# Kernel optimization log

Measured on AMD Instinct MI355X. Metric: run time of the kernel, lower is better.

The kernel has to match this reference:

```python
import jax, jax.numpy as jnp
import numpy as np

N, M, D = 500000, 128, 16

def setup_inputs() -> dict:
    key = jax.random.key(0)
    k1, k2, k3 = jax.random.split(key, 3)
    points = jax.random.uniform(k1, (N, D), dtype=jnp.float32)
    centers = jax.random.uniform(k2, (M, D), dtype=jnp.float32)
    # module initializes covs_inv_sqrt = 15*I per center; add small noise so it's non-trivial
    covs_inv_sqrt = 15.0 * jnp.eye(D, dtype=jnp.float32)[None, :, :] \
        + 0.1 * jax.random.normal(k3, (M, D, D), dtype=jnp.float32)
    weights = jnp.ones((M,), dtype=jnp.float32)
    threshold = jnp.zeros((1,), dtype=jnp.float32)
    return {"points": points, "centers": centers, "covs_inv_sqrt": covs_inv_sqrt,
            "weights": weights, "threshold": threshold}

def reference(points, centers, covs_inv_sqrt, weights, threshold):
    # refresh(): covs_inv = L @ L^T per center
    covs_inv = jnp.einsum('jde,jfe->jdf', covs_inv_sqrt, covs_inv_sqrt)  # [M,D,D]
    # equal_clusters=True branch
    w = jnp.abs(weights)
    center_prs = w / (w.sum() + 1e-30)
    coefs = center_prs * jnp.sqrt(jnp.linalg.det(covs_inv))  # [M]
    # Mahalanobis quadratic form (x-c)^T S (x-c) expanded as xSx - 2 xSc + cSc
    S_flat = covs_inv.reshape(M, D * D)                          # [M,D^2]
    xx = (points[:, :, None] * points[:, None, :]).reshape(-1, D * D)  # [N,D^2]
    Sc = jnp.einsum('jde,je->jd', covs_inv, centers)             # [M,D]
    cSc = jnp.einsum('jd,jd->j', centers, Sc)                    # [M]
    q = xx @ S_flat.T - 2.0 * (points @ Sc.T) + cSc[None, :]     # [N,M]
    d_ij = -0.5 * q
    # weighted online logsumexp over centers (KeOps logsumexp with weight Vj(coefs))
    log_lik = jax.nn.logsumexp(d_ij, axis=1, b=coefs[None, :], keepdims=True)  # [N,1]
    return log_lik - threshold
```

## Files before the change

### kernel.cpp

```cpp
#include <hip/hip_runtime.h>
#include <math.h>

#define M_CTR 128
#define D_DIM 16
#define KSTEPS 10
#define NSLOT 80
#define GRID_MAIN 2048
#define LOG2E 1.4426950408889634f
#define LN2   0.6931471805599453f

typedef _Float16 half8  __attribute__((ext_vector_type(8)));
typedef __fp16   fp16x2 __attribute__((ext_vector_type(2)));
typedef float   f32x16  __attribute__((ext_vector_type(16)));

struct SlotTab { unsigned char a[NSLOT]; unsigned char b[NSLOT]; unsigned char m[NSLOT]; };
constexpr SlotTab make_tab() {
    SlotTab T{};
    int s = 0;
    for (int d = 0; d < 8; ++d) { T.a[s] = (unsigned char)d; T.b[s] = (unsigned char)d; T.m[s] = 0; ++s; }
    for (int d = 0; d < 8; ++d)
        for (int f = d + 1; f < 8; ++f) { T.a[s] = (unsigned char)d; T.b[s] = (unsigned char)f; T.m[s] = 0; ++s; }
    for (int d = 0; d < 8; ++d)
        for (int f2 = d + 1; f2 < 8; ++f2) { T.a[s] = (unsigned char)d; T.b[s] = (unsigned char)(f2 + 8); T.m[s] = 0; ++s; }
    for (int d = 0; d < 4; ++d) { T.a[s] = (unsigned char)d; T.b[s] = (unsigned char)(d + 8); T.m[s] = 1; ++s; }
    for (int d = 0; d < 8; ++d) { T.a[s] = (unsigned char)d; T.b[s] = 0; T.m[s] = 2; ++s; }
    for (; s < NSLOT; ++s) { T.a[s] = 0; T.b[s] = 0; T.m[s] = 3; }
    return T;
}
constexpr SlotTab TAB = make_tab();

__global__ __launch_bounds__(64) void gmm_prep_kernel(
    const float* __restrict__ centers,
    const float* __restrict__ Lmat,
    const float* __restrict__ weights,
    float* __restrict__ ws)
{
    const int j    = blockIdx.x;
    const int lane = threadIdx.x;
    const int r    = lane & 15;

    __shared__ float S_lds[D_DIM][D_DIM + 1];
    __shared__ float Scp_lds[D_DIM];

    float Lr[D_DIM];
    {
        const float4* Lrow = (const float4*)(Lmat + (size_t)j * 256 + r * 16);
        #pragma unroll
        for (int q = 0; q < 4; ++q) {
            const float4 v = Lrow[q];
            Lr[q * 4 + 0] = v.x; Lr[q * 4 + 1] = v.y;
            Lr[q * 4 + 2] = v.z; Lr[q * 4 + 3] = v.w;
        }
    }

    float u[D_DIM];
    #pragma unroll
    for (int e = 0; e < D_DIM; ++e) u[e] = Lr[e];
    float logdet = 0.f;
    #pragma unroll
    for (int k = 0; k < D_DIM; ++k) {
        const float pk = __shfl(u[k], k);
        logdet += logf(fabsf(pk));
        const float f = u[k] * (1.0f / pk);
        #pragma unroll
        for (int c = k + 1; c < D_DIM; ++c) {
            const float rkc = __shfl(u[c], k);
            if (r > k) u[c] -= f * rkc;
        }
    }

    #pragma unroll
    for (int f = 0; f < D_DIM; ++f) {
        float acc = 0.f;
        #pragma unroll
        for (int e = 0; e < D_DIM; ++e) acc += Lr[e] * __shfl(Lr[e], f);
        if (lane < D_DIM) S_lds[lane][f] = acc;
    }
    __syncthreads();

    float c[D_DIM];
    {
        const float4* cc = (const float4*)(centers + (size_t)j * D_DIM);
        #pragma unroll
        for (int q = 0; q < 4; ++q) {
            const float4 v = cc[q];
            c[q * 4 + 0] = v.x - 0.5f; c[q * 4 + 1] = v.y - 0.5f;
            c[q * 4 + 2] = v.z - 0.5f; c[q * 4 + 3] = v.w - 0.5f;
        }
    }
    if (lane < D_DIM) {
        float acc = 0.f;
        #pragma unroll
        for (int f = 0; f < D_DIM; ++f) acc += S_lds[lane][f] * c[f];
        Scp_lds[lane] = acc;
    }
    __syncthreads();
    float cSc = 0.f;
    #pragma unroll
    for (int d = 0; d < D_DIM; ++d) cSc += c[d] * Scp_lds[d];

    float wa = fabsf(weights[lane]) + fabsf(weights[lane + 64]);
    #pragma unroll
    for (int off = 32; off > 0; off >>= 1) wa += __shfl_xor(wa, off);
    const float lc = logf(fabsf(weights[j])) - logf(wa + 1e-30f) + logdet;
    const float cst_half = (lc - 0.5f * cSc) * 0.5f;

    if (lane < 2 * KSTEPS) {
        const int t  = lane >> 1;
        const int hi = lane & 1;
        const int mt = j >> 5;
        half8 hv;
        for (int e = 0; e < 8; ++e) {
            const int s  = t * 8 + e;
            const int mm = TAB.m[s], a = TAB.a[s], b = TAB.b[s];
            float val;
            if (mm == 0) {
                const int d = hi ? ((a + 8) & 15) : a;
                const int f = hi ? ((b + 8) & 15) : b;
                val = (d == f) ? -0.5f * S_lds[d][d] : -S_lds[d][f];
            } else if (mm == 1) {
                const int d = a + 4 * hi, f = a + 8 + 4 * hi;
                val = -S_lds[d][f];
            } else if (mm == 2) {
                val = Scp_lds[a + 8 * hi];
            } else {
                val = (s == 76) ? cst_half : 0.f;
            }
            hv[e] = (_Float16)(val * LOG2E);
        }
        char* dst = (char*)ws + (((mt * KSTEPS + t) * 64) + hi * 32 + (j & 31)) * 16;
        *(half8*)dst = hv;
    }
}

__global__ __launch_bounds__(256) void gmm_main_kernel(
    const float* __restrict__ points,
    const float* __restrict__ wsf,
    const float* __restrict__ thr,
    float* __restrict__ out,
    int ntiles)
{
    __shared__ float4 A_lds4[2560];

    const int tid = threadIdx.x;
    const int w   = tid >> 6;
    const int l   = tid & 63;
    const int col = l & 31;
    const bool hi = (l >> 5) != 0;

    {
        const float4* src = (const float4*)wsf;
        #pragma unroll
        for (int i = 0; i < 10; ++i)
            A_lds4[i * 256 + tid] = src[i * 256 + tid];
    }
    __syncthreads();

    const half8* Ah = (const half8*)A_lds4 + l;
    const float thrv = thr[0];
    const float4* pbase = (const float4*)points;

    const int wid    = blockIdx.x * 4 + w;
    const int stride = GRID_MAIN * 4;

    const f32x16 ZV = {0.f,0.f,0.f,0.f,0.f,0.f,0.f,0.f,
                       0.f,0.f,0.f,0.f,0.f,0.f,0.f,0.f};

    for (int tile = wid; tile < ntiles; tile += stride) {
        float z[D_DIM];
        {
            const float4* px = pbase + ((size_t)tile * 32 + col) * 4;
            #pragma unroll
            for (int q = 0; q < 4; ++q) {
                const float4 v = px[q];
                z[q * 4 + 0] = v.x - 0.5f; z[q * 4 + 1] = v.y - 0.5f;
                z[q * 4 + 2] = v.z - 0.5f; z[q * 4 + 3] = v.w - 0.5f;
            }
        }

        float zs8[16], pp[4];
        #pragma unroll
        for (int i = 0; i < 16; ++i) zs8[i] = hi ? z[(i + 8) & 15] : z[i];
        #pragma unroll
        for (int i = 0; i < 4; ++i) {
            const float a = hi ? z[i + 4]  : z[i];
            const float b = hi ? z[i + 12] : z[i + 8];
            pp[i] = a * b;
        }

        f32x16 acc0, acc1, acc2, acc3;

        #pragma unroll
        for (int t = 0; t < KSTEPS; ++t) {
            float pv[8];
            #pragma unroll
            for (int e = 0; e < 8; ++e) {
                const int s  = t * 8 + e;
                const int mm = TAB.m[s], a = TAB.a[s], b = TAB.b[s];
                pv[e] = (mm == 0) ? zs8[a] * zs8[b]
                      : (mm == 1) ? pp[a]
                      : (mm == 2) ? zs8[a]
                      : ((s == 76) ? 1.0f : 0.0f);
            }
            union { half8 h8; fp16x2 h2[4]; } u;
            u.h2[0] = __builtin_amdgcn_cvt_pkrtz(pv[0], pv[1]);
            u.h2[1] = __builtin_amdgcn_cvt_pkrtz(pv[2], pv[3]);
            u.h2[2] = __builtin_amdgcn_cvt_pkrtz(pv[4], pv[5]);
            u.h2[3] = __builtin_amdgcn_cvt_pkrtz(pv[6], pv[7]);
            const half8 bf = u.h8;

            const half8 a0 = Ah[(0 * KSTEPS + t) * 64];
            const half8 a1 = Ah[(1 * KSTEPS + t) * 64];
            const half8 a2 = Ah[(2 * KSTEPS + t) * 64];
            const half8 a3 = Ah[(3 * KSTEPS + t) * 64];
            if (t == 0) {
                acc0 = __builtin_amdgcn_mfma_f32_32x32x16_f16(a0, bf, ZV, 0, 0, 0);
                acc1 = __builtin_amdgcn_mfma_f32_32x32x16_f16(a1, bf, ZV, 0, 0, 0);
                acc2 = __builtin_amdgcn_mfma_f32_32x32x16_f16(a2, bf, ZV, 0, 0, 0);
                acc3 = __builtin_amdgcn_mfma_f32_32x32x16_f16(a3, bf, ZV, 0, 0, 0);
            } else {
                acc0 = __builtin_amdgcn_mfma_f32_32x32x16_f16(a0, bf, acc0, 0, 0, 0);
                acc1 = __builtin_amdgcn_mfma_f32_32x32x16_f16(a1, bf, acc1, 0, 0, 0);
                acc2 = __builtin_amdgcn_mfma_f32_32x32x16_f16(a2, bf, acc2, 0, 0, 0);
                acc3 = __builtin_amdgcn_mfma_f32_32x32x16_f16(a3, bf, acc3, 0, 0, 0);
            }
        }

        float t0[8];
        #pragma unroll
        for (int i = 0; i < 8; ++i)
            t0[i] = fmaxf(fmaxf(acc0[i], acc0[i + 8]), fmaxf(acc1[i], acc1[i + 8]));
        #pragma unroll
        for (int i = 0; i < 8; ++i)
            t0[i] = fmaxf(t0[i], fmaxf(fmaxf(acc2[i], acc2[i + 8]), fmaxf(acc3[i], acc3[i + 8])));
        float m0 = fmaxf(fmaxf(t0[0], t0[1]), fmaxf(t0[2], t0[3]));
        float m1 = fmaxf(fmaxf(t0[4], t0[5]), fmaxf(t0[6], t0[7]));
        const float mx = fmaxf(m0, m1);

        float s0 = 0.f, s1 = 0.f, s2 = 0.f, s3 = 0.f;
        #pragma unroll
        for (int rr = 0; rr < 16; ++rr) {
            s0 += __builtin_amdgcn_exp2f(acc0[rr] - mx);
            s1 += __builtin_amdgcn_exp2f(acc1[rr] - mx);
            s2 += __builtin_amdgcn_exp2f(acc2[rr] - mx);
            s3 += __builtin_amdgcn_exp2f(acc3[rr] - mx);
        }
        float ss = (s0 + s1) + (s2 + s3);

        const float om = __shfl_xor(mx, 32);
        const float os = __shfl_xor(ss, 32);
        const float M2 = fmaxf(mx, om);
        const float S2 = ss * __builtin_amdgcn_exp2f(mx - M2)
                       + os * __builtin_amdgcn_exp2f(om - M2);

        if (l < 32)
            out[tile * 32 + l] = fmaf(LN2, M2 + __builtin_amdgcn_logf(S2), -thrv);
    }
}

extern "C" void kernel_launch(void* const* d_in, const int* in_sizes, int n_in,
                              void* d_out, int out_size, void* d_ws, size_t ws_size,
                              hipStream_t stream) {
    const float* points  = (const float*)d_in[0];
    const float* centers = (const float*)d_in[1];
    const float* covs    = (const float*)d_in[2];
    const float* weights = (const float*)d_in[3];
    const float* thr     = (const float*)d_in[4];
    float* out = (float*)d_out;
    float* ws  = (float*)d_ws;

    const int n      = in_sizes[0] / D_DIM;
    const int ntiles = n / 32;

    gmm_prep_kernel<<<M_CTR, 64, 0, stream>>>(centers, covs, weights, ws);
    gmm_main_kernel<<<GRID_MAIN, 256, 0, stream>>>(points, ws, thr, out, ntiles);
}
```

Before: 50.91 us.

## Software-pipeline MFMA compute of the next tile with the previous tile's epilogue

Restructures the per-wave tile loop into a two-stage software pipeline with double-buffered accumulators. The MFMA chain for tile n+1 is issued before the exp/logsumexp epilogue of tile n, so matrix and vector/transcendental work can overlap. The grid drops from 2048 to 512 blocks so each wave handles several tiles and the pipeline has depth. The second accumulator set doubles accumulator register use, which may lower occupancy. The smaller grid also reduces latency hiding across waves.

```diff
diff --git a/kernel.cpp b/kernel.cpp
--- a/kernel.cpp
+++ b/kernel.cpp
@@ -5,7 +5,7 @@
 #define D_DIM 16
 #define KSTEPS 10
 #define NSLOT 80
-#define GRID_MAIN 2048
+#define GRID_MAIN 512
 #define LOG2E 1.4426950408889634f
 #define LN2   0.6931471805599453f
 
@@ -133,6 +133,95 @@
     }
 }
 
+#define COMPUTE(ACC0, ACC1, ACC2, ACC3, TILE)                               \
+    do {                                                                    \
+        float z_[D_DIM];                                                    \
+        {                                                                   \
+            const float4* px_ = pbase + ((size_t)(TILE) * 32 + col) * 4;    \
+            _Pragma("unroll")                                               \
+            for (int q = 0; q < 4; ++q) {                                   \
+                const float4 v_ = px_[q];                                   \
+                z_[q * 4 + 0] = v_.x - 0.5f; z_[q * 4 + 1] = v_.y - 0.5f;   \
+                z_[q * 4 + 2] = v_.z - 0.5f; z_[q * 4 + 3] = v_.w - 0.5f;   \
+            }                                                               \
+        }                                                                   \
+        float zs_[16], zl_[4], zh_[4];                                      \
+        _Pragma("unroll")                                                   \
+        for (int i = 0; i < 16; ++i) zs_[i] = hi ? z_[(i + 8) & 15] : z_[i];\
+        _Pragma("unroll")                                                   \
+        for (int i = 0; i < 4; ++i) {                                       \
+            zl_[i] = hi ? z_[i + 4]  : z_[i];                               \
+            zh_[i] = hi ? z_[i + 12] : z_[i + 8];                           \
+        }                                                                   \
+        _Pragma("unroll")                                                   \
+        for (int t = 0; t < KSTEPS; ++t) {                                  \
+            float pv_[8];                                                   \
+            _Pragma("unroll")                                               \
+            for (int e = 0; e < 8; ++e) {                                   \
+                const int s_  = t * 8 + e;                                  \
+                const int mm_ = TAB.m[s_], a_ = TAB.a[s_], b_ = TAB.b[s_];  \
+                pv_[e] = (mm_ == 0) ? zs_[a_] * zs_[b_]                     \
+                       : (mm_ == 1) ? zl_[a_] * zh_[a_]                     \
+                       : (mm_ == 2) ? zs_[a_]                               \
+                       : ((s_ == 76) ? 1.0f : 0.0f);                        \
+            }                                                               \
+            union { half8 h8; fp16x2 h2[4]; } u_;                           \
+            u_.h2[0] = __builtin_amdgcn_cvt_pkrtz(pv_[0], pv_[1]);          \
+            u_.h2[1] = __builtin_amdgcn_cvt_pkrtz(pv_[2], pv_[3]);          \
+            u_.h2[2] = __builtin_amdgcn_cvt_pkrtz(pv_[4], pv_[5]);          \
+            u_.h2[3] = __builtin_amdgcn_cvt_pkrtz(pv_[6], pv_[7]);          \
+            const half8 bf_ = u_.h8;                                        \
+            const half8 a0_ = Ah[(0 * KSTEPS + t) * 64];                    \
+            const half8 a1_ = Ah[(1 * KSTEPS + t) * 64];                    \
+            const half8 a2_ = Ah[(2 * KSTEPS + t) * 64];                    \
+            const half8 a3_ = Ah[(3 * KSTEPS + t) * 64];                    \
+            if (t == 0) {                                                   \
+                ACC0 = __builtin_amdgcn_mfma_f32_32x32x16_f16(a0_, bf_, ZV, 0, 0, 0); \
+                ACC1 = __builtin_amdgcn_mfma_f32_32x32x16_f16(a1_, bf_, ZV, 0, 0, 0); \
+                ACC2 = __builtin_amdgcn_mfma_f32_32x32x16_f16(a2_, bf_, ZV, 0, 0, 0); \
+                ACC3 = __builtin_amdgcn_mfma_f32_32x32x16_f16(a3_, bf_, ZV, 0, 0, 0); \
+            } else {                                                        \
+                ACC0 = __builtin_amdgcn_mfma_f32_32x32x16_f16(a0_, bf_, ACC0, 0, 0, 0); \
+                ACC1 = __builtin_amdgcn_mfma_f32_32x32x16_f16(a1_, bf_, ACC1, 0, 0, 0); \
+                ACC2 = __builtin_amdgcn_mfma_f32_32x32x16_f16(a2_, bf_, ACC2, 0, 0, 0); \
+                ACC3 = __builtin_amdgcn_mfma_f32_32x32x16_f16(a3_, bf_, ACC3, 0, 0, 0); \
+            }                                                               \
+        }                                                                   \
+    } while (0)
+
+#define EPILOGUE(ACC0, ACC1, ACC2, ACC3, TIDX)                              \
+    do {                                                                    \
+        float t0_[8];                                                       \
+        _Pragma("unroll")                                                   \
+        for (int i = 0; i < 8; ++i)                                         \
+            t0_[i] = fmaxf(fmaxf(ACC0[i], ACC0[i + 8]),                     \
+                           fmaxf(ACC1[i], ACC1[i + 8]));                    \
+        _Pragma("unroll")                                                   \
+        for (int i = 0; i < 8; ++i)                                         \
+            t0_[i] = fmaxf(t0_[i], fmaxf(fmaxf(ACC2[i], ACC2[i + 8]),       \
+                                         fmaxf(ACC3[i], ACC3[i + 8])));     \
+        float m0_ = fmaxf(fmaxf(t0_[0], t0_[1]), fmaxf(t0_[2], t0_[3]));    \
+        float m1_ = fmaxf(fmaxf(t0_[4], t0_[5]), fmaxf(t0_[6], t0_[7]));    \
+        const float mx_ = fmaxf(m0_, m1_);                                  \
+        float s0_ = 0.f, s1_ = 0.f, s2_ = 0.f, s3_ = 0.f;                   \
+        _Pragma("unroll")                                                   \
+        for (int rr = 0; rr < 16; ++rr) {                                   \
+            s0_ += __builtin_amdgcn_exp2f(ACC0[rr] - mx_);                  \
+            s1_ += __builtin_amdgcn_exp2f(ACC1[rr] - mx_);                  \
+            s2_ += __builtin_amdgcn_exp2f(ACC2[rr] - mx_);                  \
+            s3_ += __builtin_amdgcn_exp2f(ACC3[rr] - mx_);                  \
+        }                                                                   \
+        float ss_ = (s0_ + s1_) + (s2_ + s3_);                              \
+        const float om_ = __shfl_xor(mx_, 32);                              \
+        const float os_ = __shfl_xor(ss_, 32);                              \
+        const float M2_ = fmaxf(mx_, om_);                                  \
+        const float S2_ = ss_ * __builtin_amdgcn_exp2f(mx_ - M2_)           \
+                        + os_ * __builtin_amdgcn_exp2f(om_ - M2_);          \
+        if (l < 32)                                                         \
+            out[(TIDX) * 32 + l] =                                          \
+                fmaf(LN2, M2_ + __builtin_amdgcn_logf(S2_), -thrv);         \
+    } while (0)
+
 __global__ __launch_bounds__(256) void gmm_main_kernel(
     const float* __restrict__ points,
     const float* __restrict__ wsf,
@@ -166,96 +255,28 @@
     const f32x16 ZV = {0.f,0.f,0.f,0.f,0.f,0.f,0.f,0.f,
                        0.f,0.f,0.f,0.f,0.f,0.f,0.f,0.f};
 
-    for (int tile = wid; tile < ntiles; tile += stride) {
-        float z[D_DIM];
-        {
-            const float4* px = pbase + ((size_t)tile * 32 + col) * 4;
-            #pragma unroll
-            for (int q = 0; q < 4; ++q) {
-                const float4 v = px[q];
-                z[q * 4 + 0] = v.x - 0.5f; z[q * 4 + 1] = v.y - 0.5f;
-                z[q * 4 + 2] = v.z - 0.5f; z[q * 4 + 3] = v.w - 0.5f;
-            }
-        }
-
-        float zs8[16], pp[4];
-        #pragma unroll
-        for (int i = 0; i < 16; ++i) zs8[i] = hi ? z[(i + 8) & 15] : z[i];
-        #pragma unroll
-        for (int i = 0; i < 4; ++i) {
-            const float a = hi ? z[i + 4]  : z[i];
-            const float b = hi ? z[i + 12] : z[i + 8];
-            pp[i] = a * b;
-        }
-
-        f32x16 acc0, acc1, acc2, acc3;
-
-        #pragma unroll
-        for (int t = 0; t < KSTEPS; ++t) {
-            float pv[8];
-            #pragma unroll
-            for (int e = 0; e < 8; ++e) {
-                const int s  = t * 8 + e;
-                const int mm = TAB.m[s], a = TAB.a[s], b = TAB.b[s];
-                pv[e] = (mm == 0) ? zs8[a] * zs8[b]
-                      : (mm == 1) ? pp[a]
-                      : (mm == 2) ? zs8[a]
-                      : ((s == 76) ? 1.0f : 0.0f);
-            }
-            union { half8 h8; fp16x2 h2[4]; } u;
-            u.h2[0] = __builtin_amdgcn_cvt_pkrtz(pv[0], pv[1]);
-            u.h2[1] = __builtin_amdgcn_cvt_pkrtz(pv[2], pv[3]);
-            u.h2[2] = __builtin_amdgcn_cvt_pkrtz(pv[4], pv[5]);
-            u.h2[3] = __builtin_amdgcn_cvt_pkrtz(pv[6], pv[7]);
-            const half8 bf = u.h8;
-
-            const half8 a0 = Ah[(0 * KSTEPS + t) * 64];
-            const half8 a1 = Ah[(1 * KSTEPS + t) * 64];
-            const half8 a2 = Ah[(2 * KSTEPS + t) * 64];
-            const half8 a3 = Ah[(3 * KSTEPS + t) * 64];
-            if (t == 0) {
-                acc0 = __builtin_amdgcn_mfma_f32_32x32x16_f16(a0, bf, ZV, 0, 0, 0);
-                acc1 = __builtin_amdgcn_mfma_f32_32x32x16_f16(a1, bf, ZV, 0, 0, 0);
-                acc2 = __builtin_amdgcn_mfma_f32_32x32x16_f16(a2, bf, ZV, 0, 0, 0);
-                acc3 = __builtin_amdgcn_mfma_f32_32x32x16_f16(a3, bf, ZV, 0, 0, 0);
-            } else {
-                acc0 = __builtin_amdgcn_mfma_f32_32x32x16_f16(a0, bf, acc0, 0, 0, 0);
-                acc1 = __builtin_amdgcn_mfma_f32_32x32x16_f16(a1, bf, acc1, 0, 0, 0);
-                acc2 = __builtin_amdgcn_mfma_f32_32x32x16_f16(a2, bf, acc2, 0, 0, 0);
-                acc3 = __builtin_amdgcn_mfma_f32_32x32x16_f16(a3, bf, acc3, 0, 0, 0);
-            }
-        }
-
-        float t0[8];
-        #pragma unroll
-        for (int i = 0; i < 8; ++i)
-            t0[i] = fmaxf(fmaxf(acc0[i], acc0[i + 8]), fmaxf(acc1[i], acc1[i + 8]));
-        #pragma unroll
-        for (int i = 0; i < 8; ++i)
-            t0[i] = fmaxf(t0[i], fmaxf(fmaxf(acc2[i], acc2[i + 8]), fmaxf(acc3[i], acc3[i + 8])));
-        float m0 = fmaxf(fmaxf(t0[0], t0[1]), fmaxf(t0[2], t0[3]));
-        float m1 = fmaxf(fmaxf(t0[4], t0[5]), fmaxf(t0[6], t0[7]));
-        const float mx = fmaxf(m0, m1);
-
-        float s0 = 0.f, s1 = 0.f, s2 = 0.f, s3 = 0.f;
-        #pragma unroll
-        for (int rr = 0; rr < 16; ++rr) {
-            s0 += __builtin_amdgcn_exp2f(acc0[rr] - mx);
-            s1 += __builtin_amdgcn_exp2f(acc1[rr] - mx);
-            s2 += __builtin_amdgcn_exp2f(acc2[rr] - mx);
-            s3 += __builtin_amdgcn_exp2f(acc3[rr] - mx);
-        }
-        float ss = (s0 + s1) + (s2 + s3);
-
-        const float om = __shfl_xor(mx, 32);
-        const float os = __shfl_xor(ss, 32);
-        const float M2 = fmaxf(mx, om);
-        const float S2 = ss * __builtin_amdgcn_exp2f(mx - M2)
-                       + os * __builtin_amdgcn_exp2f(om - M2);
-
-        if (l < 32)
-            out[tile * 32 + l] = fmaf(LN2, M2 + __builtin_amdgcn_logf(S2), -thrv);
-    }
+    f32x16 aP0, aP1, aP2, aP3;
+    f32x16 aC0, aC1, aC2, aC3;
+
+    int cur = wid;
+    if (cur >= ntiles) return;
+
+    COMPUTE(aP0, aP1, aP2, aP3, cur);
+
+    int nxt = cur + stride;
+    while (nxt < ntiles) {
+        COMPUTE(aC0, aC1, aC2, aC3, nxt);
+        EPILOGUE(aP0, aP1, aP2, aP3, cur);
+        cur = nxt; nxt += stride;
+        if (nxt >= ntiles) {
+            EPILOGUE(aC0, aC1, aC2, aC3, cur);
+            return;
+        }
+        COMPUTE(aP0, aP1, aP2, aP3, nxt);
+        EPILOGUE(aC0, aC1, aC2, aC3, cur);
+        cur = nxt; nxt += stride;
+    }
+    EPILOGUE(aP0, aP1, aP2, aP3, cur);
 }
 
 extern "C" void kernel_launch(void* const* d_in, const int* in_sizes, int n_in,
```

Result: faster. 46.36 us (-8.9%).

## Stage B fragments through LDS and use persistent 512-thread blocks

Applied to the files above, without the earlier changes.

Builds all per-tile fp16 B fragments first and stores them in a per-wave LDS region, then runs a non-unrolled MFMA loop reading A and B from LDS. The grid shrinks to 256 blocks of 512 threads. The hi half-wave now loads the point's quads in rotated order, which removes the per-element selects. The aim is lower register pressure and a cleaner MFMA issue stream, but the 120KB LDS footprint limits each CU to one block and adds LDS traffic.

```diff
diff --git a/kernel.cpp b/kernel.cpp
--- a/kernel.cpp
+++ b/kernel.cpp
@@ -5,7 +5,7 @@
 #define D_DIM 16
 #define KSTEPS 10
 #define NSLOT 80
-#define GRID_MAIN 2048
+#define GRID_MAIN 256
 #define LOG2E 1.4426950408889634f
 #define LN2   0.6931471805599453f
 
@@ -133,14 +133,47 @@
     }
 }
 
-__global__ __launch_bounds__(256) void gmm_main_kernel(
+#define EPILOGUE(ACC0, ACC1, ACC2, ACC3, TIDX)                              \
+    do {                                                                    \
+        float t0_[8];                                                       \
+        _Pragma("unroll")                                                   \
+        for (int i = 0; i < 8; ++i)                                         \
+            t0_[i] = fmaxf(fmaxf(ACC0[i], ACC0[i + 8]),                     \
+                           fmaxf(ACC1[i], ACC1[i + 8]));                    \
+        _Pragma("unroll")                                                   \
+        for (int i = 0; i < 8; ++i)                                         \
+            t0_[i] = fmaxf(t0_[i], fmaxf(fmaxf(ACC2[i], ACC2[i + 8]),       \
+                                         fmaxf(ACC3[i], ACC3[i + 8])));     \
+        float m0_ = fmaxf(fmaxf(t0_[0], t0_[1]), fmaxf(t0_[2], t0_[3]));    \
+        float m1_ = fmaxf(fmaxf(t0_[4], t0_[5]), fmaxf(t0_[6], t0_[7]));    \
+        const float mx_ = fmaxf(m0_, m1_);                                  \
+        float s0_ = 0.f, s1_ = 0.f, s2_ = 0.f, s3_ = 0.f;                   \
+        _Pragma("unroll")                                                   \
+        for (int rr = 0; rr < 16; ++rr) {                                   \
+            s0_ += __builtin_amdgcn_exp2f(ACC0[rr] - mx_);                  \
+            s1_ += __builtin_amdgcn_exp2f(ACC1[rr] - mx_);                  \
+            s2_ += __builtin_amdgcn_exp2f(ACC2[rr] - mx_);                  \
+            s3_ += __builtin_amdgcn_exp2f(ACC3[rr] - mx_);                  \
+        }                                                                   \
+        float ss_ = (s0_ + s1_) + (s2_ + s3_);                              \
+        const float om_ = __shfl_xor(mx_, 32);                              \
+        const float os_ = __shfl_xor(ss_, 32);                              \
+        const float M2_ = fmaxf(mx_, om_);                                  \
+        const float S2_ = ss_ * __builtin_amdgcn_exp2f(mx_ - M2_)           \
+                        + os_ * __builtin_amdgcn_exp2f(om_ - M2_);          \
+        if (l < 32)                                                         \
+            out[(TIDX) * 32 + l] =                                          \
+                fmaf(LN2, M2_ + __builtin_amdgcn_logf(S2_), -thrv);         \
+    } while (0)
+
+__global__ __launch_bounds__(512) void gmm_main_kernel(
     const float* __restrict__ points,
     const float* __restrict__ wsf,
     const float* __restrict__ thr,
     float* __restrict__ out,
     int ntiles)
 {
-    __shared__ float4 A_lds4[2560];
+    __shared__ float4 ldsv[7680];
 
     const int tid = threadIdx.x;
     const int w   = tid >> 6;
@@ -151,44 +184,40 @@
     {
         const float4* src = (const float4*)wsf;
         #pragma unroll
-        for (int i = 0; i < 10; ++i)
-            A_lds4[i * 256 + tid] = src[i * 256 + tid];
+        for (int i = 0; i < 5; ++i)
+            ldsv[i * 512 + tid] = src[i * 512 + tid];
     }
     __syncthreads();
 
-    const half8* Ah = (const half8*)A_lds4 + l;
-    const float thrv = thr[0];
+    const half8* Ah  = (const half8*)ldsv + l;
+    char*        Bb  = (char*)ldsv + 40960 + w * 10240 + l * 16;
+    const float  thrv = thr[0];
     const float4* pbase = (const float4*)points;
 
-    const int wid    = blockIdx.x * 4 + w;
-    const int stride = GRID_MAIN * 4;
+    const int wid    = blockIdx.x * 8 + w;
+    const int stride = GRID_MAIN * 8;
+    const int qoff   = hi ? 2 : 0;
 
     const f32x16 ZV = {0.f,0.f,0.f,0.f,0.f,0.f,0.f,0.f,
                        0.f,0.f,0.f,0.f,0.f,0.f,0.f,0.f};
 
     for (int tile = wid; tile < ntiles; tile += stride) {
-        float z[D_DIM];
+        float zs[D_DIM];
         {
             const float4* px = pbase + ((size_t)tile * 32 + col) * 4;
             #pragma unroll
             for (int q = 0; q < 4; ++q) {
-                const float4 v = px[q];
-                z[q * 4 + 0] = v.x - 0.5f; z[q * 4 + 1] = v.y - 0.5f;
-                z[q * 4 + 2] = v.z - 0.5f; z[q * 4 + 3] = v.w - 0.5f;
+                const float4 v = px[(q + qoff) & 3];
+                zs[q * 4 + 0] = v.x - 0.5f; zs[q * 4 + 1] = v.y - 0.5f;
+                zs[q * 4 + 2] = v.z - 0.5f; zs[q * 4 + 3] = v.w - 0.5f;
             }
         }
-
-        float zs8[16], pp[4];
-        #pragma unroll
-        for (int i = 0; i < 16; ++i) zs8[i] = hi ? z[(i + 8) & 15] : z[i];
+        float zl[4], zh[4];
         #pragma unroll
         for (int i = 0; i < 4; ++i) {
-            const float a = hi ? z[i + 4]  : z[i];
-            const float b = hi ? z[i + 12] : z[i + 8];
-            pp[i] = a * b;
-        }
-
-        f32x16 acc0, acc1, acc2, acc3;
+            zl[i] = hi ? zs[i + 12] : zs[i];
+            zh[i] = hi ? zs[i + 4]  : zs[i + 8];
+        }
 
         #pragma unroll
         for (int t = 0; t < KSTEPS; ++t) {
@@ -197,9 +226,9 @@
             for (int e = 0; e < 8; ++e) {
                 const int s  = t * 8 + e;
                 const int mm = TAB.m[s], a = TAB.a[s], b = TAB.b[s];
-                pv[e] = (mm == 0) ? zs8[a] * zs8[b]
-                      : (mm == 1) ? pp[a]
-                      : (mm == 2) ? zs8[a]
+                pv[e] = (mm == 0) ? zs[a] * zs[b]
+                      : (mm == 1) ? zl[a] * zh[a]
+                      : (mm == 2) ? zs[a]
                       : ((s == 76) ? 1.0f : 0.0f);
             }
             union { half8 h8; fp16x2 h2[4]; } u;
@@ -207,54 +236,31 @@
             u.h2[1] = __builtin_amdgcn_cvt_pkrtz(pv[2], pv[3]);
             u.h2[2] = __builtin_amdgcn_cvt_pkrtz(pv[4], pv[5]);
             u.h2[3] = __builtin_amdgcn_cvt_pkrtz(pv[6], pv[7]);
-            const half8 bf = u.h8;
-
+            *(half8*)(Bb + t * 1024) = u.h8;
+        }
+
+        f32x16 acc0, acc1, acc2, acc3;
+        {
+            const half8 bf = *(const half8*)(Bb + 0);
+            acc0 = __builtin_amdgcn_mfma_f32_32x32x16_f16(Ah[(0 * KSTEPS) * 64], bf, ZV, 0, 0, 0);
+            acc1 = __builtin_amdgcn_mfma_f32_32x32x16_f16(Ah[(1 * KSTEPS) * 64], bf, ZV, 0, 0, 0);
+            acc2 = __builtin_amdgcn_mfma_f32_32x32x16_f16(Ah[(2 * KSTEPS) * 64], bf, ZV, 0, 0, 0);
+            acc3 = __builtin_amdgcn_mfma_f32_32x32x16_f16(Ah[(3 * KSTEPS) * 64], bf, ZV, 0, 0, 0);
+        }
+        #pragma clang loop unroll(disable)
+        for (int t = 1; t < KSTEPS; ++t) {
+            const half8 bf = *(const half8*)(Bb + t * 1024);
             const half8 a0 = Ah[(0 * KSTEPS + t) * 64];
             const half8 a1 = Ah[(1 * KSTEPS + t) * 64];
             const half8 a2 = Ah[(2 * KSTEPS + t) * 64];
             const half8 a3 = Ah[(3 * KSTEPS + t) * 64];
-            if (t == 0) {
-                acc0 = __builtin_amdgcn_mfma_f32_32x32x16_f16(a0, bf, ZV, 0, 0, 0);
-                acc1 = __builtin_amdgcn_mfma_f32_32x32x16_f16(a1, bf, ZV, 0, 0, 0);
-                acc2 = __builtin_amdgcn_mfma_f32_32x32x16_f16(a2, bf, ZV, 0, 0, 0);
-                acc3 = __builtin_amdgcn_mfma_f32_32x32x16_f16(a3, bf, ZV, 0, 0, 0);
-            } else {
-                acc0 = __builtin_amdgcn_mfma_f32_32x32x16_f16(a0, bf, acc0, 0, 0, 0);
-                acc1 = __builtin_amdgcn_mfma_f32_32x32x16_f16(a1, bf, acc1, 0, 0, 0);
-                acc2 = __builtin_amdgcn_mfma_f32_32x32x16_f16(a2, bf, acc2, 0, 0, 0);
-                acc3 = __builtin_amdgcn_mfma_f32_32x32x16_f16(a3, bf, acc3, 0, 0, 0);
-            }
-        }
-
-        float t0[8];
-        #pragma unroll
-        for (int i = 0; i < 8; ++i)
-            t0[i] = fmaxf(fmaxf(acc0[i], acc0[i + 8]), fmaxf(acc1[i], acc1[i + 8]));
-        #pragma unroll
-        for (int i = 0; i < 8; ++i)
-            t0[i] = fmaxf(t0[i], fmaxf(fmaxf(acc2[i], acc2[i + 8]), fmaxf(acc3[i], acc3[i + 8])));
-        float m0 = fmaxf(fmaxf(t0[0], t0[1]), fmaxf(t0[2], t0[3]));
-        float m1 = fmaxf(fmaxf(t0[4], t0[5]), fmaxf(t0[6], t0[7]));
-        const float mx = fmaxf(m0, m1);
-
-        float s0 = 0.f, s1 = 0.f, s2 = 0.f, s3 = 0.f;
-        #pragma unroll
-        for (int rr = 0; rr < 16; ++rr) {
-            s0 += __builtin_amdgcn_exp2f(acc0[rr] - mx);
-            s1 += __builtin_amdgcn_exp2f(acc1[rr] - mx);
-            s2 += __builtin_amdgcn_exp2f(acc2[rr] - mx);
-            s3 += __builtin_amdgcn_exp2f(acc3[rr] - mx);
-        }
-        float ss = (s0 + s1) + (s2 + s3);
-
-        const float om = __shfl_xor(mx, 32);
-        const float os = __shfl_xor(ss, 32);
-        const float M2 = fmaxf(mx, om);
-        const float S2 = ss * __builtin_amdgcn_exp2f(mx - M2)
-                       + os * __builtin_amdgcn_exp2f(om - M2);
-
-        if (l < 32)
-            out[tile * 32 + l] = fmaf(LN2, M2 + __builtin_amdgcn_logf(S2), -thrv);
+            acc0 = __builtin_amdgcn_mfma_f32_32x32x16_f16(a0, bf, acc0, 0, 0, 0);
+            acc1 = __builtin_amdgcn_mfma_f32_32x32x16_f16(a1, bf, acc1, 0, 0, 0);
+            acc2 = __builtin_amdgcn_mfma_f32_32x32x16_f16(a2, bf, acc2, 0, 0, 0);
+            acc3 = __builtin_amdgcn_mfma_f32_32x32x16_f16(a3, bf, acc3, 0, 0, 0);
+        }
+
+        EPILOGUE(acc0, acc1, acc2, acc3, tile);
     }
 }
 
@@ -273,5 +279,5 @@
     const int ntiles = n / 32;
 
     gmm_prep_kernel<<<M_CTR, 64, 0, stream>>>(centers, covs, weights, ws);
-    gmm_main_kernel<<<GRID_MAIN, 256, 0, stream>>>(points, ws, thr, out, ntiles);
-}
+    gmm_main_kernel<<<GRID_MAIN, 512, 0, stream>>>(points, ws, thr, out, ntiles);
+}
```

After: 42.75 us. 16.0% less time.
